# Performance work log

Hardware: AMD Instinct MI355X
Metric: run time of the kernel (lower is better)

## Reference

```python
import jax, jax.numpy as jnp
import numpy as np

DIM = 1152
HEADS = 9
MID = 256
B, N = 8, 1024


def _conprefix(x, dw, db, uw, ub):
    # torch Linear: y = x @ W.T + b
    kv = jnp.tanh(x @ dw.T + db) @ uw.T + ub  # [B, N, 2*dim]
    q = jnp.zeros(kv.shape[:2] + (DIM,), kv.dtype)
    return jnp.concatenate([q, kv], axis=-1)  # [B, N, 3*dim]


def setup_inputs() -> dict:
    key = jax.random.key(0)
    ks = jax.random.split(key, 12)
    s = 0.02
    return {
        "x": jax.random.normal(ks[0], (B, N, DIM), dtype=jnp.float32),
        "Wqkv": jax.random.normal(ks[1], (3 * DIM, DIM), dtype=jnp.float32) * s,
        "Wproj": jax.random.normal(ks[2], (DIM, DIM), dtype=jnp.float32) * s,
        "bproj": jax.random.normal(ks[3], (DIM,), dtype=jnp.float32) * s,
        "down_w": jax.random.normal(ks[4], (MID, DIM), dtype=jnp.float32) * s,
        "down_b": jax.random.normal(ks[5], (MID,), dtype=jnp.float32) * s,
        "up_w": jax.random.normal(ks[6], (2 * DIM, MID), dtype=jnp.float32) * s,
        "up_b": jax.random.normal(ks[7], (2 * DIM,), dtype=jnp.float32) * s,
        "pdown_w": jax.random.normal(ks[8], (MID, DIM), dtype=jnp.float32) * s,
        "pdown_b": jax.random.normal(ks[9], (MID,), dtype=jnp.float32) * s,
        "pup_w": jax.random.normal(ks[10], (2 * DIM, MID), dtype=jnp.float32) * s,
        "pup_b": jax.random.normal(ks[11], (2 * DIM,), dtype=jnp.float32) * s,
        "task": 5,
    }


def reference(x, Wqkv, Wproj, bproj, down_w, down_b, up_w, up_b,
              pdown_w, pdown_b, pup_w, pup_b, task):
    b, n, c = x.shape
    hd = c // HEADS
    scale = hd ** (-0.5)
    qkv = x @ Wqkv.T  # [B, N, 3C] (qkv_bias=False)
    task_prefix_tensor = None
    if task <= 3:
        pass
    elif task == 4:
        qkv = qkv + _conprefix(x, down_w, down_b, up_w, up_b)
        task_prefix_tensor = down_w
    else:
        qkv = (qkv + _conprefix(x, pdown_w, pdown_b, pup_w, pup_b)
                   + _conprefix(x, down_w, down_b, up_w, up_b))
        task_prefix_tensor = down_w
    qkv = qkv.reshape(b, n, 3, HEADS, hd).transpose(2, 0, 3, 1, 4)  # [3,B,H,N,hd]
    q, k, v = qkv[0], qkv[1], qkv[2]
    attn = jax.nn.softmax(jnp.einsum('bhqd,bhkd->bhqk', q, k) * scale, axis=-1)
    out = jnp.einsum('bhqk,bhkd->bhqd', attn, v)  # [B,H,N,hd]
    out = out.transpose(0, 2, 1, 3).reshape(b, n, c)
    out = out @ Wproj.T + bproj
    return (out, task_prefix_tensor)
```

## Files before the change

### kernel.cpp

```cpp
#include <hip/hip_runtime.h>
#include <math.h>

namespace {

typedef unsigned short u16;
typedef __attribute__((ext_vector_type(8))) short short8;
typedef __attribute__((ext_vector_type(4))) float f32x4;
typedef __attribute__((ext_vector_type(16))) float f32x16;

constexpr int kDim   = 1152;
constexpr int kHeads = 9;
constexpr int kMid   = 256;
constexpr int kB     = 8;
constexpr int kN     = 1024;
constexpr int kM     = kB * kN;
constexpr int kQS    = 3584;
constexpr float kCexp  = 0.12753837360881433f;

__device__ __forceinline__ u16 f2bf(float f) {
    unsigned u = __builtin_bit_cast(unsigned, f);
    return (u16)((u + 0x7FFFu + ((u >> 16) & 1u)) >> 16);
}
__device__ __forceinline__ float bf2f(u16 h) {
    unsigned u = ((unsigned)h) << 16;
    return __builtin_bit_cast(float, u);
}

__device__ __forceinline__ void gload_lds16(const void* g, void* l) {
    __builtin_amdgcn_global_load_lds(
        (const __attribute__((address_space(1))) unsigned int*)g,
        (__attribute__((address_space(3))) unsigned int*)l,
        16, 0, 0);
}

__device__ __forceinline__ unsigned cvtpk(float a, float b) {
    unsigned r;
    asm volatile("v_cvt_pk_bf16_f32 %0, %1, %2" : "=v"(r) : "v"(a), "v"(b));
    return r;
}

__device__ __forceinline__ void halfswap(unsigned& x, unsigned& y, bool hihalf) {
    const unsigned xs = (unsigned)__shfl_xor((int)x, 32);
    const unsigned ys = (unsigned)__shfl_xor((int)y, 32);
    const unsigned nx = hihalf ? ys : x;
    const unsigned ny = hihalf ? y : xs;
    x = nx; y = ny;
}

__device__ __forceinline__ short8 build_pfrag(float p0, float p1, float p2, float p3,
                                              float p4, float p5, float p6, float p7,
                                              bool hihalf) {
    unsigned x1 = cvtpk(p0, p1), y1 = cvtpk(p4, p5);
    unsigned x2 = cvtpk(p2, p3), y2 = cvtpk(p6, p7);
    halfswap(x1, y1, hihalf);
    halfswap(x2, y2, hihalf);
    union { unsigned u[4]; short8 s; } pk;
    pk.u[0] = x1; pk.u[1] = x2; pk.u[2] = y1; pk.u[3] = y2;
    return pk.s;
}

constexpr int R0 = 2359296;
constexpr int R1 = R0 + 995328;
constexpr int R2 = R1 + 331776;
constexpr int R3 = R2 + 73728;
constexpr int R4 = R3 + 73728;
constexpr int R5 = R4 + 147456;
constexpr int R6 = R5 + 147456;
constexpr int R7 = R6 + 512;
constexpr int R8 = R7 + 2304;
constexpr int kQPart = 331776;
constexpr int kPrepGrid = R8 / 256;

__global__ __launch_bounds__(256)
void prep_all(const float* __restrict__ x, const float* __restrict__ Wqkv,
              const float* __restrict__ Wproj,
              const float* __restrict__ down_w, const float* __restrict__ pdown_w,
              const float* __restrict__ up_w, const float* __restrict__ pup_w,
              const float* __restrict__ down_b, const float* __restrict__ pdown_b,
              const float* __restrict__ up_b, const float* __restrict__ pup_b,
              const int* __restrict__ task,
              u16* __restrict__ xb, u16* __restrict__ wqkvb, u16* __restrict__ wprjb,
              u16* __restrict__ wdownb, u16* __restrict__ wupb,
              float* __restrict__ bd, float* __restrict__ bu)
{
    const int i = blockIdx.x * blockDim.x + threadIdx.x;
    auto cvt4s = [](const float* s, int j, float sc) {
        const float4 v = reinterpret_cast<const float4*>(s)[j];
        ushort4 o;
        o.x = f2bf(v.x * sc); o.y = f2bf(v.y * sc);
        o.z = f2bf(v.z * sc); o.w = f2bf(v.w * sc);
        return o;
    };
    if (i < R0) {
        reinterpret_cast<ushort4*>(xb)[i] = cvt4s(x, i, 1.f);
    } else if (i < R1) {
        const int j = i - R0;
        const float sc = (j < kQPart) ? kCexp : 1.f;
        reinterpret_cast<ushort4*>(wqkvb)[j] = cvt4s(Wqkv, j, sc);
    } else if (i < R2) {
        reinterpret_cast<ushort4*>(wprjb)[i - R1] = cvt4s(Wproj, i - R1, 1.f);
    } else if (i < R3) {
        reinterpret_cast<ushort4*>(wdownb)[i - R2] = cvt4s(down_w, i - R2, 1.f);
    } else if (i < R4) {
        reinterpret_cast<ushort4*>(wdownb)[73728 + (i - R3)] = cvt4s(pdown_w, i - R3, 1.f);
    } else if (i < R5) {
        const int j = i - R4, r = j >> 6, c = j & 63;
        reinterpret_cast<ushort4*>(wupb)[r * 128 + c] = cvt4s(up_w, j, 1.f);
    } else if (i < R6) {
        const int j = i - R5, r = j >> 6, c = j & 63;
        reinterpret_cast<ushort4*>(wupb)[r * 128 + 64 + c] = cvt4s(pup_w, j, 1.f);
    } else if (i < R7) {
        const int j = i - R6;
        bd[j] = (j < 256) ? down_b[j] : pdown_b[j - 256];
    } else {
        const int j = i - R7;
        bu[j] = up_b[j] + ((*task >= 5) ? pup_b[j] : 0.f);
    }
}

template<bool ACCUM, bool BIAS>
__global__ __launch_bounds__(512, 2)
void gemm8p(const u16* __restrict__ A, const u16* __restrict__ Bw,
            const float* __restrict__ bias, u16* __restrict__ C,
            int K, int lda, int ldb, int ldc)
{
    extern __shared__ char lds[];

    const int tid  = threadIdx.x;
    const int lane = tid & 63;
    const int wid  = tid >> 6;
    const int wm   = wid >> 2;
    const int wn   = wid & 3;
    const int bm   = blockIdx.x * 256;
    const int bn   = blockIdx.y * 256;
    const int l15  = lane & 15;
    const int kq   = lane >> 4;

    int srow[4], scol[4], sdst[4];
#pragma unroll
    for (int i = 0; i < 4; ++i) {
        const int id = i * 512 + tid;
        srow[i] = id >> 3;
        const int s = id & 7;
        scol[i] = (s ^ (srow[i] & 7)) * 8;
        sdst[i] = (i * 512 + wid * 64) * 16;
    }

    auto stage_pair = [&](int buf, int kt, int i) {
        const u16* ag = A  + (size_t)bm * lda + kt * 64;
        const u16* bg = Bw + (size_t)bn * ldb + kt * 64;
        gload_lds16(ag + (size_t)srow[i] * lda + scol[i], lds + buf * 32768 + sdst[i]);
        gload_lds16(bg + (size_t)srow[i] * ldb + scol[i], lds + 65536 + buf * 32768 + sdst[i]);
    };

    f32x4 acc[8][4] = {};
    const int nt = K >> 6;

#pragma unroll
    for (int i = 0; i < 4; ++i) stage_pair(0, 0, i);

    for (int t = 0; t < nt; ++t) {
        const char* Ab = lds + (t & 1) * 32768;
        const char* Bb = lds + 65536 + (t & 1) * 32768;
        const bool nxt = (t + 1 < nt);
        const int nb = (t + 1) & 1;

        short8 af[4], bf[4];

        auto rdA = [&](int mh, int ks) {
#pragma unroll
            for (int mi = 0; mi < 4; ++mi) {
                const int row = wm * 128 + mh * 64 + mi * 16 + l15;
                af[mi] = *reinterpret_cast<const short8*>(
                    Ab + row * 128 + (((ks * 4 + kq) ^ (row & 7)) * 16));
            }
        };
        auto rdB = [&](int ks) {
#pragma unroll
            for (int ni = 0; ni < 4; ++ni) {
                const int row = wn * 64 + ni * 16 + l15;
                bf[ni] = *reinterpret_cast<const short8*>(
                    Bb + row * 128 + (((ks * 4 + kq) ^ (row & 7)) * 16));
            }
        };
        auto mfma16 = [&](int mh) {
            asm volatile("s_waitcnt lgkmcnt(0)" ::: "memory");
            __builtin_amdgcn_sched_barrier(0);
            __builtin_amdgcn_s_setprio(1);
#pragma unroll
            for (int mi = 0; mi < 4; ++mi)
#pragma unroll
                for (int ni = 0; ni < 4; ++ni)
                    acc[mh * 4 + mi][ni] = __builtin_amdgcn_mfma_f32_16x16x32_bf16(
                        af[mi], bf[ni], acc[mh * 4 + mi][ni], 0, 0, 0);
            __builtin_amdgcn_s_setprio(0);
            asm volatile("" ::: "memory");
            __builtin_amdgcn_s_barrier();
            asm volatile("" ::: "memory");
        };

        if (nxt) { stage_pair(nb, t + 1, 0); stage_pair(nb, t + 1, 1); }
        if (nxt) asm volatile("s_waitcnt vmcnt(4)" ::: "memory");
        else     asm volatile("s_waitcnt vmcnt(0)" ::: "memory");
        __builtin_amdgcn_sched_barrier(0);
        __builtin_amdgcn_s_barrier();
        asm volatile("" ::: "memory");
        rdB(0); rdA(0, 0);
        mfma16(0);

        if (nxt) { stage_pair(nb, t + 1, 2); stage_pair(nb, t + 1, 3); }
        rdA(1, 0);
        mfma16(1);

        rdB(1); rdA(0, 1);
        mfma16(0);

        rdA(1, 1);
        mfma16(1);
    }

#pragma unroll
    for (int mg = 0; mg < 8; ++mg) {
#pragma unroll
        for (int ni = 0; ni < 4; ++ni) {
            const int col = bn + wn * 64 + ni * 16 + l15;
            const float bv = BIAS ? bias[col] : 0.f;
#pragma unroll
            for (int r = 0; r < 4; ++r) {
                const int row = bm + wm * 128 + mg * 16 + kq * 4 + r;
                float v = acc[mg][ni][r] + bv;
                u16* cp = C + (size_t)row * ldc + col;
                if (ACCUM) v += bf2f(*cp);
                *cp = f2bf(v);
            }
        }
    }
}

template<bool TANH, bool ACCUM, bool BIAS, bool OUT_BF16, bool KSEL, bool VT>
__global__ __launch_bounds__(256)
void gemm_mfma(const u16* __restrict__ A, const u16* __restrict__ Bw,
               const float* __restrict__ bias, void* __restrict__ Cv,
               u16* __restrict__ vt,
               int K, int lda, int ldb, int ldc,
               const int* __restrict__ taskp, int mintask)
{
    float gate = 1.f;
    if (taskp != nullptr && *taskp < mintask) {
        if (!VT) return;
        gate = 0.f;
    }
    if (KSEL && *taskp < 5) K = 256;

    __shared__ u16 As[2][128 * 64];
    __shared__ u16 Bs[2][128 * 64];

    const int tid  = threadIdx.x;
    const int lane = tid & 63;
    const int wv   = tid >> 6;
    const int wr   = (wv >> 1) * 64;
    const int wc   = (wv & 1) * 64;
    const int bm   = blockIdx.x * 128;
    const int bn   = blockIdx.y * 128;

    f32x4 acc[4][4] = {};

    const int srow = tid >> 3;
    const int sslt = tid & 7;

    auto stage = [&](int buf, int k0) {
        const u16* ab = A  + (size_t)bm * lda + k0;
        const u16* bb = Bw + (size_t)bn * ldb + k0;
#pragma unroll
        for (int i = 0; i < 4; ++i) {
            const int row = i * 32 + srow;
            gload_lds16(ab + (size_t)row * lda + sslt * 8,
                        (char*)&As[buf][0] + (i * 256 + (tid & 192)) * 16);
        }
#pragma unroll
        for (int i = 0; i < 4; ++i) {
            const int row = i * 32 + srow;
            gload_lds16(bb + (size_t)row * ldb + sslt * 8,
                        (char*)&Bs[buf][0] + (i * 256 + (tid & 192)) * 16);
        }
    };

    stage(0, 0);
    const int nk = K >> 6;
    for (int kt = 0; kt < nk; ++kt) {
        __syncthreads();
        if (kt + 1 < nk) stage((kt + 1) & 1, (kt + 1) * 64);
        const u16* as = &As[kt & 1][0];
        const u16* bs = &Bs[kt & 1][0];
#pragma unroll
        for (int ks = 0; ks < 2; ++ks) {
            short8 af[4], bf[4];
#pragma unroll
            for (int mi = 0; mi < 4; ++mi) {
                const int row = wr + mi * 16 + (lane & 15);
                af[mi] = *reinterpret_cast<const short8*>(as + row * 64 + ks * 32 + (lane >> 4) * 8);
            }
#pragma unroll
            for (int ni = 0; ni < 4; ++ni) {
                const int row = wc + ni * 16 + (lane & 15);
                bf[ni] = *reinterpret_cast<const short8*>(bs + row * 64 + ks * 32 + (lane >> 4) * 8);
            }
#pragma unroll
            for (int mi = 0; mi < 4; ++mi)
#pragma unroll
                for (int ni = 0; ni < 4; ++ni)
                    acc[mi][ni] = __builtin_amdgcn_mfma_f32_16x16x32_bf16(
                        af[mi], bf[ni], acc[mi][ni], 0, 0, 0);
        }
    }

#pragma unroll
    for (int mi = 0; mi < 4; ++mi) {
#pragma unroll
        for (int ni = 0; ni < 4; ++ni) {
            const int col = bn + wc + ni * 16 + (lane & 15);
            const float bv = BIAS ? bias[col] : 0.f;
            ushort4 tv;
#pragma unroll
            for (int r = 0; r < 4; ++r) {
                const int row = bm + wr + mi * 16 + (lane >> 4) * 4 + r;
                float v = gate * (acc[mi][ni][r] + bv);
                if (TANH) v = tanhf(v);
                if (OUT_BF16) {
                    u16* cp = (u16*)Cv + (size_t)row * ldc + col;
                    if (ACCUM) v += bf2f(*cp);
                    const u16 bb = f2bf(v);
                    *cp = bb;
                    if (VT) (&tv.x)[r] = bb;
                } else {
                    float* cp = (float*)Cv + (size_t)row * ldc + col;
                    if (ACCUM) v += *cp;
                    *cp = v;
                }
            }
            if (VT && col >= 1152) {
                const int hh = (col - 1152) >> 7;
                const int d  = (col - 1152) & 127;
                const int row0 = bm + wr + mi * 16 + (lane >> 4) * 4;
                const int bb_  = row0 >> 10;
                const int tok  = row0 & 1023;
                *reinterpret_cast<ushort4*>(
                    vt + ((size_t)(bb_ * kHeads + hh) * 128 + d) * kN + tok) = tv;
            }
        }
    }
}

__global__ __launch_bounds__(256)
void attn_mfma(const u16* __restrict__ qkv, const u16* __restrict__ vt,
               u16* __restrict__ out)
{
    __shared__ u16 Ks[2][32 * 128];
    __shared__ u16 Vs[2][128 * 32];

    const int bh = blockIdx.x, b = bh / kHeads, h = bh - b * kHeads;
    const int tid = threadIdx.x, lane = tid & 63, wv = tid >> 6;
    const int lo5 = lane & 31;
    const bool hihalf = (lane >= 32);
    const int hi = hihalf ? 1 : 0;
    const int qh = wv >> 1;
    const int kh = wv & 1;
    const int q0 = blockIdx.y * 64 + qh * 32;

    const u16* qp = qkv + (size_t)(b * kN + q0 + lo5) * kQS + h * 128;
    short8 qf[8];
#pragma unroll
    for (int f = 0; f < 8; ++f)
        qf[f] = *reinterpret_cast<const short8*>(qp + f * 16 + hi * 8);

    int koff[2], voff[2];
#pragma unroll
    for (int j = 0; j < 2; ++j) {
        const int I = j * 256 + tid;
        const int tok = I >> 4, s = I & 15;
        koff[j] = tok * kQS + ((s ^ (tok & 7)) * 8);
        const int d = I >> 2, sv = I & 3;
        voff[j] = d * kN + ((sv ^ (d & 3)) * 8);
    }
    const u16* kbase = qkv + (size_t)b * kN * kQS + kDim + h * 128;
    const u16* vbase = vt + (size_t)bh * 128 * kN;

    uint4 kr0, kr1, kr2, kr3, vr0, vr1, vr2, vr3;
    auto ldregs = [&](int t) {
        const int kt0 = t * 32, kt1 = 512 + t * 32;
        kr0 = *reinterpret_cast<const uint4*>(kbase + (size_t)kt0 * kQS + koff[0]);
        kr1 = *reinterpret_cast<const uint4*>(kbase + (size_t)kt0 * kQS + koff[1]);
        kr2 = *reinterpret_cast<const uint4*>(kbase + (size_t)kt1 * kQS + koff[0]);
        kr3 = *reinterpret_cast<const uint4*>(kbase + (size_t)kt1 * kQS + koff[1]);
        vr0 = *reinterpret_cast<const uint4*>(vbase + kt0 + voff[0]);
        vr1 = *reinterpret_cast<const uint4*>(vbase + kt0 + voff[1]);
        vr2 = *reinterpret_cast<const uint4*>(vbase + kt1 + voff[0]);
        vr3 = *reinterpret_cast<const uint4*>(vbase + kt1 + voff[1]);
    };
    auto stlds = [&]() {
        *reinterpret_cast<uint4*>((char*)&Ks[0][0] + (0 * 256 + wv * 64 + lane) * 16) = kr0;
        *reinterpret_cast<uint4*>((char*)&Ks[0][0] + (1 * 256 + wv * 64 + lane) * 16) = kr1;
        *reinterpret_cast<uint4*>((char*)&Ks[1][0] + (0 * 256 + wv * 64 + lane) * 16) = kr2;
        *reinterpret_cast<uint4*>((char*)&Ks[1][0] + (1 * 256 + wv * 64 + lane) * 16) = kr3;
        *reinterpret_cast<uint4*>((char*)&Vs[0][0] + (0 * 256 + wv * 64 + lane) * 16) = vr0;
        *reinterpret_cast<uint4*>((char*)&Vs[0][0] + (1 * 256 + wv * 64 + lane) * 16) = vr1;
        *reinterpret_cast<uint4*>((char*)&Vs[1][0] + (0 * 256 + wv * 64 + lane) * 16) = vr2;
        *reinterpret_cast<uint4*>((char*)&Vs[1][0] + (1 * 256 + wv * 64 + lane) * 16) = vr3;
    };

    f32x16 o[4] = {};
    float l = 0.f;

    ldregs(0);
    stlds();
    __syncthreads();

    for (int t = 0; t < 16; ++t) {
        if (t + 1 < 16) ldregs(t + 1);

        const char* ks = (const char*)&Ks[kh][0];
        const char* vs = (const char*)&Vs[kh][0];

        f32x16 s0 = {};
        __builtin_amdgcn_s_setprio(1);
#pragma unroll
        for (int f = 0; f < 8; ++f) {
            const short8 ka = *reinterpret_cast<const short8*>(
                ks + lo5 * 256 + (((f * 2 + hi) * 16) ^ ((lo5 & 7) << 4)));
            s0 = __builtin_amdgcn_mfma_f32_32x32x16_bf16(ka, qf[f], s0, 0, 0, 0);
        }
        __builtin_amdgcn_s_setprio(0);

        float rsum = 0.f;
#pragma unroll
        for (int r = 0; r < 16; ++r) { s0[r] = exp2f(s0[r]); rsum += s0[r]; }
        rsum += __shfl_xor(rsum, 32);
        l += rsum;

        short8 pf[2];
        pf[0] = build_pfrag(s0[0], s0[1], s0[2], s0[3], s0[4], s0[5], s0[6], s0[7], hihalf);
        pf[1] = build_pfrag(s0[8], s0[9], s0[10], s0[11], s0[12], s0[13], s0[14], s0[15], hihalf);

        __builtin_amdgcn_s_setprio(1);
#pragma unroll
        for (int dt = 0; dt < 4; ++dt) {
            const int drow = dt * 32 + lo5;
#pragma unroll
            for (int c = 0; c < 2; ++c) {
                const short8 va = *reinterpret_cast<const short8*>(
                    vs + drow * 64 + (((c * 2 + hi) * 16) ^ ((drow & 3) << 4)));
                o[dt] = __builtin_amdgcn_mfma_f32_32x32x16_bf16(va, pf[c], o[dt], 0, 0, 0);
            }
        }
        __builtin_amdgcn_s_setprio(0);

        __syncthreads();
        if (t + 1 < 16) stlds();
        __syncthreads();
    }

    char* exch = (char*)&Ks[0][0];
    float* ls  = (float*)&Vs[0][0];
    if (kh == 1) {
#pragma unroll
        for (int dt = 0; dt < 4; ++dt) {
#pragma unroll
            for (int rg = 0; rg < 4; ++rg) {
                const int kb = (dt * 4 + rg) * 8;
                ushort4 w;
                w.x = f2bf(o[dt][rg * 4 + 0]);
                w.y = f2bf(o[dt][rg * 4 + 1]);
                w.z = f2bf(o[dt][rg * 4 + 2]);
                w.w = f2bf(o[dt][rg * 4 + 3]);
                *reinterpret_cast<ushort4*>(
                    exch + qh * 8192 + lane * 128 + (kb ^ ((lane & 7) << 3))) = w;
            }
        }
        if (!hihalf) ls[qh * 32 + lo5] = l;
    }
    __syncthreads();
    if (kh == 0) {
        const float inv = 1.f / (l + ls[qh * 32 + lo5]);
        u16* op = out + (size_t)(b * kN + q0 + lo5) * kDim + h * 128;
#pragma unroll
        for (int dt = 0; dt < 4; ++dt) {
#pragma unroll
            for (int rg = 0; rg < 4; ++rg) {
                const int kb = (dt * 4 + rg) * 8;
                const ushort4 pv = *reinterpret_cast<const ushort4*>(
                    exch + qh * 8192 + lane * 128 + (kb ^ ((lane & 7) << 3)));
                const int d0 = dt * 32 + rg * 8 + hi * 4;
                ushort4 v;
                v.x = f2bf((o[dt][rg * 4 + 0] + bf2f(pv.x)) * inv);
                v.y = f2bf((o[dt][rg * 4 + 1] + bf2f(pv.y)) * inv);
                v.z = f2bf((o[dt][rg * 4 + 2] + bf2f(pv.z)) * inv);
                v.w = f2bf((o[dt][rg * 4 + 3] + bf2f(pv.w)) * inv);
                *reinterpret_cast<ushort4*>(op + d0) = v;
            }
        }
    }
}

}

extern "C" void kernel_launch(void* const* d_in, const int* in_sizes, int n_in,
                              void* d_out, int out_size, void* d_ws, size_t ws_size,
                              hipStream_t stream)
{
    const float* x       = (const float*)d_in[0];
    const float* Wqkv    = (const float*)d_in[1];
    const float* Wproj   = (const float*)d_in[2];
    const float* bproj   = (const float*)d_in[3];
    const float* down_w  = (const float*)d_in[4];
    const float* down_b  = (const float*)d_in[5];
    const float* up_w    = (const float*)d_in[6];
    const float* up_b    = (const float*)d_in[7];
    const float* pdown_w = (const float*)d_in[8];
    const float* pdown_b = (const float*)d_in[9];
    const float* pup_w   = (const float*)d_in[10];
    const float* pup_b   = (const float*)d_in[11];
    const int*   task    = (const int*)d_in[12];

    u16* xb_vt  = (u16*)d_ws;
    u16* wqkvb  = xb_vt  + (size_t)kM * kDim;
    u16* wprjb  = wqkvb  + (size_t)kQS * kDim;
    u16* wdownb = wprjb  + (size_t)kDim * kDim;
    u16* wupb   = wdownb + (size_t)512 * kDim;
    u16* h12    = wupb   + (size_t)2304 * 512;
    u16* qkvb   = h12    + (size_t)kM * 512;
    u16* aob    = qkvb   + (size_t)kM * kQS;
    float* bd   = (float*)(aob + (size_t)kM * kDim);
    float* bu   = bd + 512;
    float* out  = (float*)d_out;
    u16* xb = xb_vt;
    u16* vt = xb_vt;

    prep_all<<<kPrepGrid, 256, 0, stream>>>(
        x, Wqkv, Wproj, down_w, pdown_w, up_w, pup_w,
        down_b, pdown_b, up_b, pup_b, task,
        xb, wqkvb, wprjb, wdownb, wupb, bd, bu);

    hipFuncSetAttribute(reinterpret_cast<const void*>(&gemm8p<false, false>),
                        hipFuncAttributeMaxDynamicSharedMemorySize, 131072);

    gemm_mfma<true, false, true, true, false, false><<<dim3(kM / 128, 4), 256, 0, stream>>>(
        xb, wdownb, bd, h12, nullptr, kDim, kDim, kDim, 512, nullptr, 0);
    gemm8p<false, false><<<dim3(kM / 256, kQS / 256), 512, 131072, stream>>>(
        xb, wqkvb, nullptr, qkvb, kDim, kDim, kDim, kQS);
    gemm_mfma<false, true, true, true, true, true><<<dim3(kM / 128, 18), 256, 0, stream>>>(
        h12, wupb, bu, qkvb + kDim, vt, 512, 512, 512, kQS, task, 4);

    attn_mfma<<<dim3(kB * kHeads, kN / 64), 256, 0, stream>>>(qkvb, vt, aob);

    gemm_mfma<false, false, true, false, false, false><<<dim3(kM / 128, 9), 256, 0, stream>>>(
        aob, wprjb, bproj, out, nullptr, kDim, kDim, kDim, kDim, nullptr, 0);

    hipMemcpyAsync(out + (size_t)kM * kDim, down_w,
                   (size_t)kMid * kDim * sizeof(float),
                   hipMemcpyDeviceToDevice, stream);
}
```

Measured before the change: 337.9 us.

## Load attention K/V tiles directly from global into LDS, dropping register staging

Replaces the register-staged K/V prefetch in the attention loop (global to registers during compute, then registers to LDS) with direct global-to-LDS loads at the start of each iteration, bracketed by barriers. This frees the eight uint4 staging registers and removes the separate LDS store instructions, which may help register pressure or occupancy. In exchange, loads for the next tile no longer overlap the current tile's MFMA work, so each iteration pays the memory latency unless other waves hide it.

```diff
diff --git a/kernel.cpp b/kernel.cpp
--- a/kernel.cpp
+++ b/kernel.cpp
@@ -385,38 +385,23 @@
     const u16* kbase = qkv + (size_t)b * kN * kQS + kDim + h * 128;
     const u16* vbase = vt + (size_t)bh * 128 * kN;
 
-    uint4 kr0, kr1, kr2, kr3, vr0, vr1, vr2, vr3;
-    auto ldregs = [&](int t) {
-        const int kt0 = t * 32, kt1 = 512 + t * 32;
-        kr0 = *reinterpret_cast<const uint4*>(kbase + (size_t)kt0 * kQS + koff[0]);
-        kr1 = *reinterpret_cast<const uint4*>(kbase + (size_t)kt0 * kQS + koff[1]);
-        kr2 = *reinterpret_cast<const uint4*>(kbase + (size_t)kt1 * kQS + koff[0]);
-        kr3 = *reinterpret_cast<const uint4*>(kbase + (size_t)kt1 * kQS + koff[1]);
-        vr0 = *reinterpret_cast<const uint4*>(vbase + kt0 + voff[0]);
-        vr1 = *reinterpret_cast<const uint4*>(vbase + kt0 + voff[1]);
-        vr2 = *reinterpret_cast<const uint4*>(vbase + kt1 + voff[0]);
-        vr3 = *reinterpret_cast<const uint4*>(vbase + kt1 + voff[1]);
-    };
-    auto stlds = [&]() {
-        *reinterpret_cast<uint4*>((char*)&Ks[0][0] + (0 * 256 + wv * 64 + lane) * 16) = kr0;
-        *reinterpret_cast<uint4*>((char*)&Ks[0][0] + (1 * 256 + wv * 64 + lane) * 16) = kr1;
-        *reinterpret_cast<uint4*>((char*)&Ks[1][0] + (0 * 256 + wv * 64 + lane) * 16) = kr2;
-        *reinterpret_cast<uint4*>((char*)&Ks[1][0] + (1 * 256 + wv * 64 + lane) * 16) = kr3;
-        *reinterpret_cast<uint4*>((char*)&Vs[0][0] + (0 * 256 + wv * 64 + lane) * 16) = vr0;
-        *reinterpret_cast<uint4*>((char*)&Vs[0][0] + (1 * 256 + wv * 64 + lane) * 16) = vr1;
-        *reinterpret_cast<uint4*>((char*)&Vs[1][0] + (0 * 256 + wv * 64 + lane) * 16) = vr2;
-        *reinterpret_cast<uint4*>((char*)&Vs[1][0] + (1 * 256 + wv * 64 + lane) * 16) = vr3;
-    };
-
     f32x16 o[4] = {};
     float l = 0.f;
 
-    ldregs(0);
-    stlds();
-    __syncthreads();
-
     for (int t = 0; t < 16; ++t) {
-        if (t + 1 < 16) ldregs(t + 1);
+        __syncthreads();
+#pragma unroll
+        for (int hh = 0; hh < 2; ++hh) {
+            const int kt = hh * 512 + t * 32;
+#pragma unroll
+            for (int j = 0; j < 2; ++j) {
+                gload_lds16(kbase + (size_t)kt * kQS + koff[j],
+                            (char*)&Ks[hh][0] + (j * 256 + wv * 64) * 16);
+                gload_lds16(vbase + kt + voff[j],
+                            (char*)&Vs[hh][0] + (j * 256 + wv * 64) * 16);
+            }
+        }
+        __syncthreads();
 
         const char* ks = (const char*)&Ks[kh][0];
         const char* vs = (const char*)&Vs[kh][0];
@@ -453,12 +438,9 @@
             }
         }
         __builtin_amdgcn_s_setprio(0);
-
-        __syncthreads();
-        if (t + 1 < 16) stlds();
-        __syncthreads();
-    }
-
+    }
+
+    __syncthreads();
     char* exch = (char*)&Ks[0][0];
     float* ls  = (float*)&Vs[0][0];
     if (kh == 1) {
```

After: 327.6 us. -3.0%, faster.
